# Optimization experiments

Measured on AMD Instinct MI355X. Metric: run time of the kernel, lower is better.

Reference implementation:

```python
import jax, jax.numpy as jnp
import numpy as np

SEQ, B, H2 = 4096, 64, 256  # seq_len, batch, 2*hidden_size


def setup_inputs() -> dict:
    key = jax.random.key(0)
    k0, k1, k2, k3 = jax.random.split(key, 4)
    uni = lambda k, shape: jax.random.uniform(k, shape, jnp.float32, -0.1, 0.1)
    return {
        "encoder_outputs": jax.random.normal(k0, (SEQ, B, H2), jnp.float32),
        "weight_W_word": uni(k1, (H2, H2)),
        "bias_word": uni(k2, (H2, 1)),
        "weight_proj_word": uni(k3, (H2, 1)),
    }


def reference(encoder_outputs, weight_W_word, bias_word, weight_proj_word):
    # tanh(x @ W + b): [seq, batch, 2H]
    squish = jnp.tanh(
        jnp.einsum("sbd,de->sbe", encoder_outputs, weight_W_word)
        + bias_word[:, 0]
    )
    # projection to scalar score per (seq, batch): [seq, batch]
    attn = jnp.einsum("sbe,e->sb", squish, weight_proj_word[:, 0])
    # softmax over seq dim (original: softmax on [batch, seq] over dim 1)
    attn_norm = jax.nn.softmax(attn.T, axis=1)  # [batch, seq]
    # weighted sum over seq: [1, batch, 2H]
    vectors = jnp.einsum("sb,sbd->bd", attn_norm.T, encoder_outputs)[None]
    return (vectors, attn_norm)
```

## Files before the change

### kernel.cpp

```cpp
#include <hip/hip_runtime.h>
#include <hip/hip_bf16.h>

#define SEQ 4096
#define NB 64
#define H2 256
#define MROWS (SEQ * NB)

typedef short bf16x8 __attribute__((ext_vector_type(8)));
typedef int   i32x4  __attribute__((ext_vector_type(4)));
typedef float f32x4  __attribute__((ext_vector_type(4)));

__device__ __forceinline__ float fast_tanh(float x) {
    float e = __expf(2.0f * x);
    return 1.0f - 2.0f * __builtin_amdgcn_rcpf(e + 1.0f);
}

__global__ __launch_bounds__(256)
void pack_w_kernel(const float* __restrict__ W, __hip_bfloat16* __restrict__ Wp) {
    int t = blockIdx.x * 256 + threadIdx.x;
    int l  = t & 63;
    int n  = (t >> 6) & 15;
    int kk = t >> 10;
    int e  = n * 16 + (l & 15);
    int d0 = kk * 32 + 8 * (l >> 4);
    union { __hip_bfloat16 h[8]; i32x4 v; } cv;
#pragma unroll
    for (int i = 0; i < 8; ++i) cv.h[i] = __float2bfloat16(W[(d0 + i) * H2 + e]);
    *reinterpret_cast<i32x4*>(&Wp[(size_t)t * 8]) = cv.v;
}

__global__ __launch_bounds__(256, 2)
void logits_kernel(const float* __restrict__ enc,
                   const __hip_bfloat16* __restrict__ Wp,
                   const float* __restrict__ bias,
                   const float* __restrict__ proj,
                   float* __restrict__ attnS) {
    __shared__ __hip_bfloat16 wT[2][8192];

    const int tid   = threadIdx.x;
    const int lane  = tid & 63;
    const int w     = tid >> 6;
    const int rloc  = lane & 15;
    const int kslot = lane >> 4;
    const long r0   = (long)blockIdx.x * 128;
    const long rowA = r0 + w * 32 + rloc;

    f32x4 acc[2][16];
#pragma unroll
    for (int rt = 0; rt < 2; ++rt)
#pragma unroll
        for (int n = 0; n < 16; ++n) acc[rt][n] = (f32x4)(0.0f);

#pragma unroll
    for (int j = 0; j < 4; ++j) {
        i32x4 v = *reinterpret_cast<const i32x4*>(Wp + j * 2048 + tid * 8);
        *reinterpret_cast<i32x4*>(&wT[0][j * 2048 + tid * 8]) = v;
    }
    __syncthreads();

    int buf = 0;
#pragma unroll
    for (int kk = 0; kk < 8; ++kk) {
        i32x4 wv[4];
        if (kk < 7) {
#pragma unroll
            for (int j = 0; j < 4; ++j)
                wv[j] = *reinterpret_cast<const i32x4*>(
                    Wp + (size_t)(kk + 1) * 8192 + j * 2048 + tid * 8);
        }
        bf16x8 af[2];
#pragma unroll
        for (int rt = 0; rt < 2; ++rt) {
            const float* ap = enc + (size_t)(rowA + rt * 16) * H2 + kk * 32 + kslot * 8;
            float4 a0 = *reinterpret_cast<const float4*>(ap);
            float4 a1 = *reinterpret_cast<const float4*>(ap + 4);
            union { __hip_bfloat16 h[8]; bf16x8 v; } cv;
            cv.h[0] = __float2bfloat16(a0.x); cv.h[1] = __float2bfloat16(a0.y);
            cv.h[2] = __float2bfloat16(a0.z); cv.h[3] = __float2bfloat16(a0.w);
            cv.h[4] = __float2bfloat16(a1.x); cv.h[5] = __float2bfloat16(a1.y);
            cv.h[6] = __float2bfloat16(a1.z); cv.h[7] = __float2bfloat16(a1.w);
            af[rt] = cv.v;
        }
#pragma unroll
        for (int n = 0; n < 16; ++n) {
            bf16x8 bv = *reinterpret_cast<const bf16x8*>(&wT[buf][n * 512 + lane * 8]);
            acc[0][n] = __builtin_amdgcn_mfma_f32_16x16x32_bf16(af[0], bv, acc[0][n], 0, 0, 0);
            acc[1][n] = __builtin_amdgcn_mfma_f32_16x16x32_bf16(af[1], bv, acc[1][n], 0, 0, 0);
        }
        if (kk < 7) {
#pragma unroll
            for (int j = 0; j < 4; ++j)
                *reinterpret_cast<i32x4*>(&wT[buf ^ 1][j * 2048 + tid * 8]) = wv[j];
        }
        __syncthreads();
        buf ^= 1;
    }

    float biasv[16], projv[16];
#pragma unroll
    for (int n = 0; n < 16; ++n) {
        int e = n * 16 + rloc;
        biasv[n] = bias[e];
        projv[n] = proj[e];
    }
#pragma unroll
    for (int rt = 0; rt < 2; ++rt) {
        float pv[4];
#pragma unroll
        for (int r = 0; r < 4; ++r) {
            float p = 0.0f;
#pragma unroll
            for (int n = 0; n < 16; ++n) {
                p += projv[n] * fast_tanh(acc[rt][n][r] + biasv[n]);
            }
            p += __shfl_xor(p, 1);
            p += __shfl_xor(p, 2);
            p += __shfl_xor(p, 4);
            p += __shfl_xor(p, 8);
            pv[r] = p;
        }
        if (rloc == 0) {
            long orow = r0 + w * 32 + rt * 16 + kslot * 4;
            float4 o; o.x = pv[0]; o.y = pv[1]; o.z = pv[2]; o.w = pv[3];
            *reinterpret_cast<float4*>(&attnS[orow]) = o;
        }
    }
}

__global__ void r20_softmax(const float* __restrict__ attnS,
                            float* __restrict__ out_attn) {
    __shared__ float sL[SEQ];
    __shared__ float red[256];
    const int b = blockIdx.x;
    const int t = threadIdx.x;

    float lm = -1e30f;
    for (int s = t; s < SEQ; s += 256) {
        float v = attnS[(size_t)s * NB + b];
        sL[s] = v;
        lm = fmaxf(lm, v);
    }
    red[t] = lm;
    __syncthreads();
    for (int h = 128; h > 0; h >>= 1) {
        if (t < h) red[t] = fmaxf(red[t], red[t + h]);
        __syncthreads();
    }
    const float gmax = red[0];
    __syncthreads();

    float ls = 0.0f;
    for (int s = t; s < SEQ; s += 256) {
        float e = __expf(sL[s] - gmax);
        sL[s] = e;
        ls += e;
    }
    red[t] = ls;
    __syncthreads();
    for (int h = 128; h > 0; h >>= 1) {
        if (t < h) red[t] += red[t + h];
        __syncthreads();
    }
    const float inv = 1.0f / red[0];

    for (int s = t; s < SEQ; s += 256) {
        out_attn[(size_t)b * SEQ + s] = sL[s] * inv;
    }
}

__global__ __launch_bounds__(256)
void r20_wsum(const float* __restrict__ enc,
              const float* __restrict__ out_attn,
              float* __restrict__ partials) {
    __shared__ float wl[256];
    __shared__ float4 pf[4][64];
    const int b  = blockIdx.x & 63;
    const int c  = blockIdx.x >> 6;
    const int t  = threadIdx.x;
    const int dq = t & 63;
    const int sq = t >> 6;

    wl[t] = out_attn[(size_t)b * SEQ + c * 256 + t];
    __syncthreads();

    float4 acc = make_float4(0.f, 0.f, 0.f, 0.f);
    const size_t base = ((size_t)(c * 256 + sq * 64) * NB + b) * H2 + dq * 4;
#pragma unroll 4
    for (int j = 0; j < 64; ++j) {
        float wv = wl[sq * 64 + j];
        float4 ev = *reinterpret_cast<const float4*>(&enc[base + (size_t)j * NB * H2]);
        acc.x = fmaf(wv, ev.x, acc.x);
        acc.y = fmaf(wv, ev.y, acc.y);
        acc.z = fmaf(wv, ev.z, acc.z);
        acc.w = fmaf(wv, ev.w, acc.w);
    }
    pf[sq][dq] = acc;
    __syncthreads();
    if (sq == 0) {
        float4 a = pf[0][dq], b1 = pf[1][dq], c1 = pf[2][dq], d1 = pf[3][dq];
        float4 o;
        o.x = a.x + b1.x + c1.x + d1.x;
        o.y = a.y + b1.y + c1.y + d1.y;
        o.z = a.z + b1.z + c1.z + d1.z;
        o.w = a.w + b1.w + c1.w + d1.w;
        *reinterpret_cast<float4*>(&partials[((size_t)c * NB + b) * H2 + dq * 4]) = o;
    }
}

__global__ void r20_reduce(const float* __restrict__ partials,
                           float* __restrict__ out_vec) {
    const int b = blockIdx.x;
    const int t = threadIdx.x;
    float a = 0.0f;
    for (int c = 0; c < 16; ++c)
        a += partials[((size_t)c * NB + b) * H2 + t];
    out_vec[(size_t)b * H2 + t] = a;
}

extern "C" void kernel_launch(void* const* d_in, const int* in_sizes, int n_in,
                              void* d_out, int out_size, void* d_ws, size_t ws_size,
                              hipStream_t stream) {
    const float* enc  = (const float*)d_in[0];
    const float* W    = (const float*)d_in[1];
    const float* bias = (const float*)d_in[2];
    const float* proj = (const float*)d_in[3];

    float* out      = (float*)d_out;
    float* out_vec  = out;
    float* out_attn = out + NB * H2;

    char* ws = (char*)d_ws;
    __hip_bfloat16* Wp = (__hip_bfloat16*)ws;
    float* attnS    = (float*)(ws + 131072);
    float* partials = (float*)(ws + 131072 + (1u << 20));

    hipLaunchKernelGGL(pack_w_kernel,  dim3(32),          dim3(256), 0, stream,
                       W, Wp);
    hipLaunchKernelGGL(logits_kernel,  dim3(MROWS / 128), dim3(256), 0, stream,
                       enc, Wp, bias, proj, attnS);
    hipLaunchKernelGGL(r20_softmax,    dim3(NB),          dim3(256), 0, stream,
                       attnS, out_attn);
    hipLaunchKernelGGL(r20_wsum,       dim3(16 * NB),     dim3(256), 0, stream,
                       enc, out_attn, partials);
    hipLaunchKernelGGL(r20_reduce,     dim3(NB),          dim3(256), 0, stream,
                       partials, out_vec);
}
```

Before: 155.6 us.

## Fuse logits, softmax numerator and weighted sum into one pass over encoder

Replaces the separate logits, softmax, weighted-sum and reduce kernels with one fused kernel. Each block stages a tile of 64 sequence rows for one batch into shared memory as bf16, computes the logits with MFMA, exponentiates them without max subtraction, and accumulates both the exp sum and the exp-weighted sum of the staged rows. A small combine kernel then normalises. This reads the encoder once instead of twice. In exchange the weighted sum uses bf16-rounded inputs, the exponentials can overflow without the max shift, every tile reloads the full W from global memory, and the grid shrinks to 512 blocks.

```diff
diff --git a/kernel.cpp b/kernel.cpp
--- a/kernel.cpp
+++ b/kernel.cpp
@@ -4,7 +4,6 @@
 #define SEQ 4096
 #define NB 64
 #define H2 256
-#define MROWS (SEQ * NB)
 
 typedef short bf16x8 __attribute__((ext_vector_type(8)));
 typedef int   i32x4  __attribute__((ext_vector_type(4)));
@@ -30,71 +29,27 @@
 }
 
 __global__ __launch_bounds__(256, 2)
-void logits_kernel(const float* __restrict__ enc,
-                   const __hip_bfloat16* __restrict__ Wp,
-                   const float* __restrict__ bias,
-                   const float* __restrict__ proj,
-                   float* __restrict__ attnS) {
+void fused_kernel(const float* __restrict__ enc,
+                  const __hip_bfloat16* __restrict__ Wp,
+                  const float* __restrict__ bias,
+                  const float* __restrict__ proj,
+                  float* __restrict__ logits,
+                  float* __restrict__ vec_p,
+                  float* __restrict__ l_p) {
+    __shared__ __hip_bfloat16 aT[64][264];
     __shared__ __hip_bfloat16 wT[2][8192];
+    __shared__ float lbuf[64];
 
     const int tid   = threadIdx.x;
     const int lane  = tid & 63;
     const int w     = tid >> 6;
     const int rloc  = lane & 15;
     const int kslot = lane >> 4;
-    const long r0   = (long)blockIdx.x * 128;
-    const long rowA = r0 + w * 32 + rloc;
-
-    f32x4 acc[2][16];
-#pragma unroll
-    for (int rt = 0; rt < 2; ++rt)
-#pragma unroll
-        for (int n = 0; n < 16; ++n) acc[rt][n] = (f32x4)(0.0f);
-
-#pragma unroll
-    for (int j = 0; j < 4; ++j) {
-        i32x4 v = *reinterpret_cast<const i32x4*>(Wp + j * 2048 + tid * 8);
-        *reinterpret_cast<i32x4*>(&wT[0][j * 2048 + tid * 8]) = v;
-    }
-    __syncthreads();
-
-    int buf = 0;
-#pragma unroll
-    for (int kk = 0; kk < 8; ++kk) {
-        i32x4 wv[4];
-        if (kk < 7) {
-#pragma unroll
-            for (int j = 0; j < 4; ++j)
-                wv[j] = *reinterpret_cast<const i32x4*>(
-                    Wp + (size_t)(kk + 1) * 8192 + j * 2048 + tid * 8);
-        }
-        bf16x8 af[2];
-#pragma unroll
-        for (int rt = 0; rt < 2; ++rt) {
-            const float* ap = enc + (size_t)(rowA + rt * 16) * H2 + kk * 32 + kslot * 8;
-            float4 a0 = *reinterpret_cast<const float4*>(ap);
-            float4 a1 = *reinterpret_cast<const float4*>(ap + 4);
-            union { __hip_bfloat16 h[8]; bf16x8 v; } cv;
-            cv.h[0] = __float2bfloat16(a0.x); cv.h[1] = __float2bfloat16(a0.y);
-            cv.h[2] = __float2bfloat16(a0.z); cv.h[3] = __float2bfloat16(a0.w);
-            cv.h[4] = __float2bfloat16(a1.x); cv.h[5] = __float2bfloat16(a1.y);
-            cv.h[6] = __float2bfloat16(a1.z); cv.h[7] = __float2bfloat16(a1.w);
-            af[rt] = cv.v;
-        }
-#pragma unroll
-        for (int n = 0; n < 16; ++n) {
-            bf16x8 bv = *reinterpret_cast<const bf16x8*>(&wT[buf][n * 512 + lane * 8]);
-            acc[0][n] = __builtin_amdgcn_mfma_f32_16x16x32_bf16(af[0], bv, acc[0][n], 0, 0, 0);
-            acc[1][n] = __builtin_amdgcn_mfma_f32_16x16x32_bf16(af[1], bv, acc[1][n], 0, 0, 0);
-        }
-        if (kk < 7) {
-#pragma unroll
-            for (int j = 0; j < 4; ++j)
-                *reinterpret_cast<i32x4*>(&wT[buf ^ 1][j * 2048 + tid * 8]) = wv[j];
-        }
-        __syncthreads();
-        buf ^= 1;
-    }
+    const int b     = blockIdx.x & 63;
+    const int c     = blockIdx.x >> 6;
+
+    const int ar   = tid >> 2;
+    const int dseg = (tid & 3) * 64;
 
     float biasv[16], projv[16];
 #pragma unroll
@@ -103,16 +58,75 @@
         biasv[n] = bias[e];
         projv[n] = proj[e];
     }
-#pragma unroll
-    for (int rt = 0; rt < 2; ++rt) {
+
+    float vacc = 0.0f;
+    float lsum = 0.0f;
+
+    for (int t = 0; t < 8; ++t) {
+        const int s0 = c * 512 + t * 64;
+        __syncthreads();
+
+        {
+            const float* src = enc + ((size_t)(s0 + ar) * NB + b) * H2 + dseg;
+            float4 v[16];
+#pragma unroll
+            for (int i = 0; i < 16; ++i)
+                v[i] = *reinterpret_cast<const float4*>(src + i * 4);
+#pragma unroll
+            for (int j = 0; j < 8; ++j) {
+                union { __hip_bfloat16 h[8]; uint4 u; } cv;
+                float4 va = v[2 * j], vb = v[2 * j + 1];
+                cv.h[0] = __float2bfloat16(va.x); cv.h[1] = __float2bfloat16(va.y);
+                cv.h[2] = __float2bfloat16(va.z); cv.h[3] = __float2bfloat16(va.w);
+                cv.h[4] = __float2bfloat16(vb.x); cv.h[5] = __float2bfloat16(vb.y);
+                cv.h[6] = __float2bfloat16(vb.z); cv.h[7] = __float2bfloat16(vb.w);
+                *reinterpret_cast<uint4*>(&aT[ar][dseg + 8 * j]) = cv.u;
+            }
+        }
+#pragma unroll
+        for (int j = 0; j < 4; ++j) {
+            i32x4 v = *reinterpret_cast<const i32x4*>(Wp + j * 2048 + tid * 8);
+            *reinterpret_cast<i32x4*>(&wT[0][j * 2048 + tid * 8]) = v;
+        }
+        __syncthreads();
+
+        f32x4 acc[16];
+#pragma unroll
+        for (int n = 0; n < 16; ++n) acc[n] = (f32x4)(0.0f);
+
+        int buf = 0;
+#pragma unroll
+        for (int kk = 0; kk < 8; ++kk) {
+            i32x4 wv[4];
+            if (kk < 7) {
+#pragma unroll
+                for (int j = 0; j < 4; ++j)
+                    wv[j] = *reinterpret_cast<const i32x4*>(
+                        Wp + (size_t)(kk + 1) * 8192 + j * 2048 + tid * 8);
+            }
+            bf16x8 af = *reinterpret_cast<const bf16x8*>(
+                &aT[w * 16 + rloc][kk * 32 + kslot * 8]);
+#pragma unroll
+            for (int n = 0; n < 16; ++n) {
+                bf16x8 bv = *reinterpret_cast<const bf16x8*>(&wT[buf][n * 512 + lane * 8]);
+                acc[n] = __builtin_amdgcn_mfma_f32_16x16x32_bf16(af, bv, acc[n], 0, 0, 0);
+            }
+            if (kk < 7) {
+#pragma unroll
+                for (int j = 0; j < 4; ++j)
+                    *reinterpret_cast<i32x4*>(&wT[buf ^ 1][j * 2048 + tid * 8]) = wv[j];
+            }
+            __syncthreads();
+            buf ^= 1;
+        }
+
         float pv[4];
 #pragma unroll
         for (int r = 0; r < 4; ++r) {
             float p = 0.0f;
 #pragma unroll
-            for (int n = 0; n < 16; ++n) {
-                p += projv[n] * fast_tanh(acc[rt][n][r] + biasv[n]);
-            }
+            for (int n = 0; n < 16; ++n)
+                p += projv[n] * fast_tanh(acc[n][r] + biasv[n]);
             p += __shfl_xor(p, 1);
             p += __shfl_xor(p, 2);
             p += __shfl_xor(p, 4);
@@ -120,101 +134,50 @@
             pv[r] = p;
         }
         if (rloc == 0) {
-            long orow = r0 + w * 32 + rt * 16 + kslot * 4;
+            int rbase = w * 16 + kslot * 4;
             float4 o; o.x = pv[0]; o.y = pv[1]; o.z = pv[2]; o.w = pv[3];
-            *reinterpret_cast<float4*>(&attnS[orow]) = o;
+            *reinterpret_cast<float4*>(&logits[(size_t)b * SEQ + s0 + rbase]) = o;
+            float4 e;
+            e.x = __expf(pv[0]); e.y = __expf(pv[1]);
+            e.z = __expf(pv[2]); e.w = __expf(pv[3]);
+            *reinterpret_cast<float4*>(&lbuf[rbase]) = e;
+        }
+        __syncthreads();
+
+#pragma unroll 8
+        for (int r = 0; r < 64; ++r) {
+            float pe = lbuf[r];
+            lsum += pe;
+            vacc = fmaf(pe, __bfloat162float(aT[r][tid]), vacc);
         }
     }
-}
-
-__global__ void r20_softmax(const float* __restrict__ attnS,
-                            float* __restrict__ out_attn) {
-    __shared__ float sL[SEQ];
-    __shared__ float red[256];
+
+    vec_p[((size_t)c * NB + b) * H2 + tid] = vacc;
+    if (tid == 0) l_p[c * NB + b] = lsum;
+}
+
+__global__ __launch_bounds__(256)
+void combine_kernel(const float* __restrict__ logits,
+                    const float* __restrict__ vec_p,
+                    const float* __restrict__ l_p,
+                    float* __restrict__ out_vec,
+                    float* __restrict__ out_attn) {
     const int b = blockIdx.x;
     const int t = threadIdx.x;
 
-    float lm = -1e30f;
+    float l = 0.0f;
+#pragma unroll
+    for (int c = 0; c < 8; ++c) l += l_p[c * NB + b];
+
+    float v = 0.0f;
+#pragma unroll
+    for (int c = 0; c < 8; ++c) v += vec_p[((size_t)c * NB + b) * H2 + t];
+    const float invl = 1.0f / l;
+    out_vec[(size_t)b * H2 + t] = v * invl;
+
     for (int s = t; s < SEQ; s += 256) {
-        float v = attnS[(size_t)s * NB + b];
-        sL[s] = v;
-        lm = fmaxf(lm, v);
+        out_attn[(size_t)b * SEQ + s] = __expf(logits[(size_t)b * SEQ + s]) * invl;
     }
-    red[t] = lm;
-    __syncthreads();
-    for (int h = 128; h > 0; h >>= 1) {
-        if (t < h) red[t] = fmaxf(red[t], red[t + h]);
-        __syncthreads();
-    }
-    const float gmax = red[0];
-    __syncthreads();
-
-    float ls = 0.0f;
-    for (int s = t; s < SEQ; s += 256) {
-        float e = __expf(sL[s] - gmax);
-        sL[s] = e;
-        ls += e;
-    }
-    red[t] = ls;
-    __syncthreads();
-    for (int h = 128; h > 0; h >>= 1) {
-        if (t < h) red[t] += red[t + h];
-        __syncthreads();
-    }
-    const float inv = 1.0f / red[0];
-
-    for (int s = t; s < SEQ; s += 256) {
-        out_attn[(size_t)b * SEQ + s] = sL[s] * inv;
-    }
-}
-
-__global__ __launch_bounds__(256)
-void r20_wsum(const float* __restrict__ enc,
-              const float* __restrict__ out_attn,
-              float* __restrict__ partials) {
-    __shared__ float wl[256];
-    __shared__ float4 pf[4][64];
-    const int b  = blockIdx.x & 63;
-    const int c  = blockIdx.x >> 6;
-    const int t  = threadIdx.x;
-    const int dq = t & 63;
-    const int sq = t >> 6;
-
-    wl[t] = out_attn[(size_t)b * SEQ + c * 256 + t];
-    __syncthreads();
-
-    float4 acc = make_float4(0.f, 0.f, 0.f, 0.f);
-    const size_t base = ((size_t)(c * 256 + sq * 64) * NB + b) * H2 + dq * 4;
-#pragma unroll 4
-    for (int j = 0; j < 64; ++j) {
-        float wv = wl[sq * 64 + j];
-        float4 ev = *reinterpret_cast<const float4*>(&enc[base + (size_t)j * NB * H2]);
-        acc.x = fmaf(wv, ev.x, acc.x);
-        acc.y = fmaf(wv, ev.y, acc.y);
-        acc.z = fmaf(wv, ev.z, acc.z);
-        acc.w = fmaf(wv, ev.w, acc.w);
-    }
-    pf[sq][dq] = acc;
-    __syncthreads();
-    if (sq == 0) {
-        float4 a = pf[0][dq], b1 = pf[1][dq], c1 = pf[2][dq], d1 = pf[3][dq];
-        float4 o;
-        o.x = a.x + b1.x + c1.x + d1.x;
-        o.y = a.y + b1.y + c1.y + d1.y;
-        o.z = a.z + b1.z + c1.z + d1.z;
-        o.w = a.w + b1.w + c1.w + d1.w;
-        *reinterpret_cast<float4*>(&partials[((size_t)c * NB + b) * H2 + dq * 4]) = o;
-    }
-}
-
-__global__ void r20_reduce(const float* __restrict__ partials,
-                           float* __restrict__ out_vec) {
-    const int b = blockIdx.x;
-    const int t = threadIdx.x;
-    float a = 0.0f;
-    for (int c = 0; c < 16; ++c)
-        a += partials[((size_t)c * NB + b) * H2 + t];
-    out_vec[(size_t)b * H2 + t] = a;
 }
 
 extern "C" void kernel_launch(void* const* d_in, const int* in_sizes, int n_in,
@@ -231,17 +194,13 @@
 
     char* ws = (char*)d_ws;
     __hip_bfloat16* Wp = (__hip_bfloat16*)ws;
-    float* attnS    = (float*)(ws + 131072);
-    float* partials = (float*)(ws + 131072 + (1u << 20));
-
-    hipLaunchKernelGGL(pack_w_kernel,  dim3(32),          dim3(256), 0, stream,
-                       W, Wp);
-    hipLaunchKernelGGL(logits_kernel,  dim3(MROWS / 128), dim3(256), 0, stream,
-                       enc, Wp, bias, proj, attnS);
-    hipLaunchKernelGGL(r20_softmax,    dim3(NB),          dim3(256), 0, stream,
-                       attnS, out_attn);
-    hipLaunchKernelGGL(r20_wsum,       dim3(16 * NB),     dim3(256), 0, stream,
-                       enc, out_attn, partials);
-    hipLaunchKernelGGL(r20_reduce,     dim3(NB),          dim3(256), 0, stream,
-                       partials, out_vec);
-}
+    float* logits = (float*)(ws + 131072);
+    float* vec_p  = (float*)(ws + 131072 + (1u << 20));
+    float* l_p    = (float*)(ws + 131072 + (1u << 20) + 524288);
+
+    hipLaunchKernelGGL(pack_w_kernel,  dim3(32),  dim3(256), 0, stream, W, Wp);
+    hipLaunchKernelGGL(fused_kernel,   dim3(512), dim3(256), 0, stream,
+                       enc, Wp, bias, proj, logits, vec_p, l_p);
+    hipLaunchKernelGGL(combine_kernel, dim3(NB),  dim3(256), 0, stream,
+                       logits, vec_p, l_p, out_vec, out_attn);
+}
```

New measurement: 153.5 us. Within noise of the previous version (-1.3%).

## Stage A tile through LDS with coalesced loads, shrink logits tile, split wsum finer

Applied to the files above, without the earlier changes.

The logits kernel now loads each encoder tile with coalesced float4 reads, converts it to bf16 into a double-buffered LDS tile, and reads MFMA A-fragments from LDS. Previously each lane did strided 32-byte row reads directly from global memory. The block tile drops from 128 to 64 rows, which halves the accumulators and raises the occupancy target to 3 blocks per SM. The weighted-sum kernel splits the sequence into 32 chunks instead of 16 for more parallelism, and the reduce kernel sums 32 partials. The trade-off is twice the partials traffic, plus W being restaged in LDS for twice as many blocks.

```diff
diff --git a/kernel.cpp b/kernel.cpp
--- a/kernel.cpp
+++ b/kernel.cpp
@@ -29,12 +29,13 @@
     *reinterpret_cast<i32x4*>(&Wp[(size_t)t * 8]) = cv.v;
 }
 
-__global__ __launch_bounds__(256, 2)
+__global__ __launch_bounds__(256, 3)
 void logits_kernel(const float* __restrict__ enc,
                    const __hip_bfloat16* __restrict__ Wp,
                    const float* __restrict__ bias,
                    const float* __restrict__ proj,
                    float* __restrict__ attnS) {
+    __shared__ __hip_bfloat16 aT[2][64][40];
     __shared__ __hip_bfloat16 wT[2][8192];
 
     const int tid   = threadIdx.x;
@@ -42,52 +43,61 @@
     const int w     = tid >> 6;
     const int rloc  = lane & 15;
     const int kslot = lane >> 4;
-    const long r0   = (long)blockIdx.x * 128;
-    const long rowA = r0 + w * 32 + rloc;
-
-    f32x4 acc[2][16];
-#pragma unroll
-    for (int rt = 0; rt < 2; ++rt)
-#pragma unroll
-        for (int n = 0; n < 16; ++n) acc[rt][n] = (f32x4)(0.0f);
-
-#pragma unroll
-    for (int j = 0; j < 4; ++j) {
-        i32x4 v = *reinterpret_cast<const i32x4*>(Wp + j * 2048 + tid * 8);
-        *reinterpret_cast<i32x4*>(&wT[0][j * 2048 + tid * 8]) = v;
+    const long r0   = (long)blockIdx.x * 64;
+
+    const int ar0 = tid >> 3;
+    const int ad0 = (tid & 7) * 4;
+    const int ar1 = (tid + 256) >> 3;
+    const int ad1 = ad0;
+
+    f32x4 acc[16];
+#pragma unroll
+    for (int n = 0; n < 16; ++n) acc[n] = (f32x4)(0.0f);
+
+    {
+        float4 v0 = *reinterpret_cast<const float4*>(&enc[(r0 + ar0) * H2 + ad0]);
+        float4 v1 = *reinterpret_cast<const float4*>(&enc[(r0 + ar1) * H2 + ad1]);
+        union { __hip_bfloat16 h[4]; uint2 u; } c0, c1;
+        c0.h[0] = __float2bfloat16(v0.x); c0.h[1] = __float2bfloat16(v0.y);
+        c0.h[2] = __float2bfloat16(v0.z); c0.h[3] = __float2bfloat16(v0.w);
+        c1.h[0] = __float2bfloat16(v1.x); c1.h[1] = __float2bfloat16(v1.y);
+        c1.h[2] = __float2bfloat16(v1.z); c1.h[3] = __float2bfloat16(v1.w);
+        *reinterpret_cast<uint2*>(&aT[0][ar0][ad0]) = c0.u;
+        *reinterpret_cast<uint2*>(&aT[0][ar1][ad1]) = c1.u;
+#pragma unroll
+        for (int j = 0; j < 4; ++j) {
+            i32x4 v = *reinterpret_cast<const i32x4*>(Wp + j * 2048 + tid * 8);
+            *reinterpret_cast<i32x4*>(&wT[0][j * 2048 + tid * 8]) = v;
+        }
     }
     __syncthreads();
 
     int buf = 0;
 #pragma unroll
     for (int kk = 0; kk < 8; ++kk) {
-        i32x4 wv[4];
+        float4 v0, v1; i32x4 wv[4];
         if (kk < 7) {
+            v0 = *reinterpret_cast<const float4*>(&enc[(r0 + ar0) * H2 + (kk + 1) * 32 + ad0]);
+            v1 = *reinterpret_cast<const float4*>(&enc[(r0 + ar1) * H2 + (kk + 1) * 32 + ad1]);
 #pragma unroll
             for (int j = 0; j < 4; ++j)
                 wv[j] = *reinterpret_cast<const i32x4*>(
                     Wp + (size_t)(kk + 1) * 8192 + j * 2048 + tid * 8);
         }
-        bf16x8 af[2];
-#pragma unroll
-        for (int rt = 0; rt < 2; ++rt) {
-            const float* ap = enc + (size_t)(rowA + rt * 16) * H2 + kk * 32 + kslot * 8;
-            float4 a0 = *reinterpret_cast<const float4*>(ap);
-            float4 a1 = *reinterpret_cast<const float4*>(ap + 4);
-            union { __hip_bfloat16 h[8]; bf16x8 v; } cv;
-            cv.h[0] = __float2bfloat16(a0.x); cv.h[1] = __float2bfloat16(a0.y);
-            cv.h[2] = __float2bfloat16(a0.z); cv.h[3] = __float2bfloat16(a0.w);
-            cv.h[4] = __float2bfloat16(a1.x); cv.h[5] = __float2bfloat16(a1.y);
-            cv.h[6] = __float2bfloat16(a1.z); cv.h[7] = __float2bfloat16(a1.w);
-            af[rt] = cv.v;
-        }
+        bf16x8 af = *reinterpret_cast<const bf16x8*>(&aT[buf][w * 16 + rloc][kslot * 8]);
 #pragma unroll
         for (int n = 0; n < 16; ++n) {
             bf16x8 bv = *reinterpret_cast<const bf16x8*>(&wT[buf][n * 512 + lane * 8]);
-            acc[0][n] = __builtin_amdgcn_mfma_f32_16x16x32_bf16(af[0], bv, acc[0][n], 0, 0, 0);
-            acc[1][n] = __builtin_amdgcn_mfma_f32_16x16x32_bf16(af[1], bv, acc[1][n], 0, 0, 0);
+            acc[n] = __builtin_amdgcn_mfma_f32_16x16x32_bf16(af, bv, acc[n], 0, 0, 0);
         }
         if (kk < 7) {
+            union { __hip_bfloat16 h[4]; uint2 u; } c0, c1;
+            c0.h[0] = __float2bfloat16(v0.x); c0.h[1] = __float2bfloat16(v0.y);
+            c0.h[2] = __float2bfloat16(v0.z); c0.h[3] = __float2bfloat16(v0.w);
+            c1.h[0] = __float2bfloat16(v1.x); c1.h[1] = __float2bfloat16(v1.y);
+            c1.h[2] = __float2bfloat16(v1.z); c1.h[3] = __float2bfloat16(v1.w);
+            *reinterpret_cast<uint2*>(&aT[buf ^ 1][ar0][ad0]) = c0.u;
+            *reinterpret_cast<uint2*>(&aT[buf ^ 1][ar1][ad1]) = c1.u;
 #pragma unroll
             for (int j = 0; j < 4; ++j)
                 *reinterpret_cast<i32x4*>(&wT[buf ^ 1][j * 2048 + tid * 8]) = wv[j];
@@ -103,31 +113,27 @@
         biasv[n] = bias[e];
         projv[n] = proj[e];
     }
-#pragma unroll
-    for (int rt = 0; rt < 2; ++rt) {
-        float pv[4];
-#pragma unroll
-        for (int r = 0; r < 4; ++r) {
-            float p = 0.0f;
-#pragma unroll
-            for (int n = 0; n < 16; ++n) {
-                p += projv[n] * fast_tanh(acc[rt][n][r] + biasv[n]);
-            }
-            p += __shfl_xor(p, 1);
-            p += __shfl_xor(p, 2);
-            p += __shfl_xor(p, 4);
-            p += __shfl_xor(p, 8);
-            pv[r] = p;
-        }
-        if (rloc == 0) {
-            long orow = r0 + w * 32 + rt * 16 + kslot * 4;
-            float4 o; o.x = pv[0]; o.y = pv[1]; o.z = pv[2]; o.w = pv[3];
-            *reinterpret_cast<float4*>(&attnS[orow]) = o;
-        }
-    }
-}
-
-__global__ void r20_softmax(const float* __restrict__ attnS,
+    float pv[4];
+#pragma unroll
+    for (int r = 0; r < 4; ++r) {
+        float p = 0.0f;
+#pragma unroll
+        for (int n = 0; n < 16; ++n)
+            p += projv[n] * fast_tanh(acc[n][r] + biasv[n]);
+        p += __shfl_xor(p, 1);
+        p += __shfl_xor(p, 2);
+        p += __shfl_xor(p, 4);
+        p += __shfl_xor(p, 8);
+        pv[r] = p;
+    }
+    if (rloc == 0) {
+        long orow = r0 + w * 16 + kslot * 4;
+        float4 o; o.x = pv[0]; o.y = pv[1]; o.z = pv[2]; o.w = pv[3];
+        *reinterpret_cast<float4*>(&attnS[orow]) = o;
+    }
+}
+
+__global__ void r22_softmax(const float* __restrict__ attnS,
                             float* __restrict__ out_attn) {
     __shared__ float sL[SEQ];
     __shared__ float red[256];
@@ -169,10 +175,10 @@
 }
 
 __global__ __launch_bounds__(256)
-void r20_wsum(const float* __restrict__ enc,
+void r22_wsum(const float* __restrict__ enc,
               const float* __restrict__ out_attn,
               float* __restrict__ partials) {
-    __shared__ float wl[256];
+    __shared__ float wl[128];
     __shared__ float4 pf[4][64];
     const int b  = blockIdx.x & 63;
     const int c  = blockIdx.x >> 6;
@@ -180,14 +186,14 @@
     const int dq = t & 63;
     const int sq = t >> 6;
 
-    wl[t] = out_attn[(size_t)b * SEQ + c * 256 + t];
+    if (t < 128) wl[t] = out_attn[(size_t)b * SEQ + c * 128 + t];
     __syncthreads();
 
     float4 acc = make_float4(0.f, 0.f, 0.f, 0.f);
-    const size_t base = ((size_t)(c * 256 + sq * 64) * NB + b) * H2 + dq * 4;
+    const size_t base = ((size_t)(c * 128 + sq * 32) * NB + b) * H2 + dq * 4;
 #pragma unroll 4
-    for (int j = 0; j < 64; ++j) {
-        float wv = wl[sq * 64 + j];
+    for (int j = 0; j < 32; ++j) {
+        float wv = wl[sq * 32 + j];
         float4 ev = *reinterpret_cast<const float4*>(&enc[base + (size_t)j * NB * H2]);
         acc.x = fmaf(wv, ev.x, acc.x);
         acc.y = fmaf(wv, ev.y, acc.y);
@@ -207,12 +213,13 @@
     }
 }
 
-__global__ void r20_reduce(const float* __restrict__ partials,
+__global__ void r22_reduce(const float* __restrict__ partials,
                            float* __restrict__ out_vec) {
     const int b = blockIdx.x;
     const int t = threadIdx.x;
     float a = 0.0f;
-    for (int c = 0; c < 16; ++c)
+#pragma unroll
+    for (int c = 0; c < 32; ++c)
         a += partials[((size_t)c * NB + b) * H2 + t];
     out_vec[(size_t)b * H2 + t] = a;
 }
@@ -234,14 +241,14 @@
     float* attnS    = (float*)(ws + 131072);
     float* partials = (float*)(ws + 131072 + (1u << 20));
 
-    hipLaunchKernelGGL(pack_w_kernel,  dim3(32),          dim3(256), 0, stream,
+    hipLaunchKernelGGL(pack_w_kernel,  dim3(32),         dim3(256), 0, stream,
                        W, Wp);
-    hipLaunchKernelGGL(logits_kernel,  dim3(MROWS / 128), dim3(256), 0, stream,
+    hipLaunchKernelGGL(logits_kernel,  dim3(MROWS / 64), dim3(256), 0, stream,
                        enc, Wp, bias, proj, attnS);
-    hipLaunchKernelGGL(r20_softmax,    dim3(NB),          dim3(256), 0, stream,
+    hipLaunchKernelGGL(r22_softmax,    dim3(NB),         dim3(256), 0, stream,
                        attnS, out_attn);
-    hipLaunchKernelGGL(r20_wsum,       dim3(16 * NB),     dim3(256), 0, stream,
+    hipLaunchKernelGGL(r22_wsum,       dim3(32 * NB),    dim3(256), 0, stream,
                        enc, out_attn, partials);
-    hipLaunchKernelGGL(r20_reduce,     dim3(NB),          dim3(256), 0, stream,
+    hipLaunchKernelGGL(r22_reduce,     dim3(NB),         dim3(256), 0, stream,
                        partials, out_vec);
 }
```

Result: faster. 149.3 us (-4.0%).
